# Kernel optimization log

Hardware: AMD Instinct MI355X
Metric: run time of the kernel (lower is better)

The kernel has to match this reference:

```python
import jax, jax.numpy as jnp
import numpy as np

INC, OUTC, NHEADS, KSIZE = 256, 256, 8, 5


def setup_inputs() -> dict:
    key = jax.random.key(0)
    k1, k2 = jax.random.split(key, 2)
    x = jax.random.normal(k1, (4, INC, 64, 64), dtype=jnp.float32)
    w_qkv = jax.random.normal(k2, (3 * OUTC, INC), dtype=jnp.float32) * 0.02
    b_qkv = jnp.zeros((3 * OUTC,), dtype=jnp.float32)
    return {"x": x, "w_qkv": w_qkv, "b_qkv": b_qkv}


def reference(x, w_qkv, b_qkv):
    N, Cin, H, W = x.shape
    hd = OUTC // NHEADS
    ofs = KSIZE // 2
    K2 = KSIZE * KSIZE

    # 1x1 conv == pointwise matmul over channels
    qkv = jnp.einsum('nchw,dc->ndhw', x, w_qkv) + b_qkv[None, :, None, None]
    Q = qkv[:, :OUTC]
    K = qkv[:, OUTC:2 * OUTC]
    V = qkv[:, 2 * OUTC:]

    # Zero-pad K/V; track validity so boundary softmax only spans in-bounds
    # positions (the torch code slices smaller windows at borders -> no pad
    # contribution to softmax).
    Kp = jnp.pad(K, ((0, 0), (0, 0), (ofs, ofs), (ofs, ofs)))
    Vp = jnp.pad(V, ((0, 0), (0, 0), (ofs, ofs), (ofs, ofs)))
    valid = jnp.pad(jnp.ones((H, W), dtype=bool), ((ofs, ofs), (ofs, ofs)))

    # Sliding windows via KSIZE^2 static shifted slices: [N,D,H,W,K2]
    k_win = jnp.stack([Kp[:, :, dy:dy + H, dx:dx + W]
                       for dy in range(KSIZE) for dx in range(KSIZE)], axis=-1)
    v_win = jnp.stack([Vp[:, :, dy:dy + H, dx:dx + W]
                       for dy in range(KSIZE) for dx in range(KSIZE)], axis=-1)
    m_win = jnp.stack([valid[dy:dy + H, dx:dx + W]
                       for dy in range(KSIZE) for dx in range(KSIZE)], axis=-1)  # [H,W,K2]

    qh = Q.reshape(N, NHEADS, hd, H, W)
    kh = k_win.reshape(N, NHEADS, hd, H, W, K2)
    vh = v_win.reshape(N, NHEADS, hd, H, W, K2)

    scores = jnp.einsum('ngdhw,ngdhwk->nghwk', qh, kh)          # [N,G,H,W,K2]
    scores = jnp.where(m_win[None, None], scores, -jnp.inf)
    att = jax.nn.softmax(scores, axis=-1)
    out = jnp.einsum('nghwk,ngdhwk->ngdhw', att, vh)            # [N,G,hd,H,W]
    return out.reshape(N, OUTC, H, W)
```

## Files before the change

### kernel.cpp

```cpp
#include <hip/hip_runtime.h>
#include <hip/hip_bf16.h>
#include <math.h>

#define CIN 256
#define COUT 768
#define OUTC 256
#define HH 64
#define WW 64
#define HW 4096

typedef unsigned int uint32;
typedef unsigned short ushort16;
typedef unsigned long long u64;

using short8 = __attribute__((ext_vector_type(8))) short;
using f32x4  = __attribute__((ext_vector_type(4))) float;
using hf2    = __attribute__((ext_vector_type(2))) _Float16;

__device__ inline uint32 pkbf2(float a, float b) {
    __hip_bfloat162 h = __float22bfloat162_rn(make_float2(a, b));
    union { __hip_bfloat162 h2; uint32 u; } cv; cv.h2 = h;
    return cv.u;
}
__device__ inline uint32 pkhf2(float a, float b) {
    union { _Float16 h[2]; uint32 u; } cv;
    cv.h[0] = (_Float16)a; cv.h[1] = (_Float16)b;
    return cv.u;
}
__device__ inline float dpp_xor1(float x) {
#if __has_builtin(__builtin_amdgcn_update_dpp)
    int i = __builtin_amdgcn_update_dpp(0, __float_as_int(x),
                                        0xB1, 0xF, 0xF, true);
    return __int_as_float(i);
#else
    return __shfl_xor(x, 1, 64);
#endif
}
__device__ inline float dot2acc(hf2 a, hf2 b, float c) {
#if __has_builtin(__builtin_amdgcn_fdot2)
    return __builtin_amdgcn_fdot2(a, b, c, false);
#else
    c = fmaf((float)a[0], (float)b[0], c);
    return fmaf((float)a[1], (float)b[1], c);
#endif
}

#define LDSTR 40

__global__ __launch_bounds__(256) void qkv_gemm_kernel(
    const float* __restrict__ x, const float* __restrict__ wq,
    const float* __restrict__ bq, ushort16* __restrict__ qkv)
{
    __shared__ __align__(16) char smem[32768];
    ushort16* As = (ushort16*)smem;
    ushort16* Bs = (ushort16*)smem + 128 * LDSTR;

    const int n   = blockIdx.z;
    const int d0  = blockIdx.y * 128;
    const int p0  = blockIdx.x * 128;
    const int tid = threadIdx.x;
    const int lane = tid & 63;
    const int wid  = tid >> 6;
    const int wm = wid >> 1;
    const int wn = wid & 1;

    const float* xb = x + (size_t)n * CIN * HW;

    const int arow = tid >> 2;
    const int akk  = (tid & 3) * 8;
    const float* aptr = wq + (size_t)(d0 + arow) * CIN + akk;
    const int bkg = (tid >> 6) * 8;
    const int bpg = (tid & 63) * 2;
    const float* bptr = xb + (size_t)bkg * HW + p0 + bpg;

    ushort16* awr0 = &As[arow * LDSTR + akk];
    ushort16* awr1 = &As[(arow + 64) * LDSTR + akk];
    ushort16* bwr0 = &Bs[bpg * LDSTR + bkg];
    ushort16* bwr1 = &Bs[(bpg + 1) * LDSTR + bkg];

    f32x4 acc[4][4];
    #pragma unroll
    for (int i = 0; i < 4; ++i)
        #pragma unroll
        for (int j = 0; j < 4; ++j) acc[i][j] = (f32x4){0.f, 0.f, 0.f, 0.f};

    const int lrow = lane & 15;
    const int lk   = (lane >> 4) * 8;

    float4 a0[4], a1[4];
    float2 b0[8], b1[8];

#define LOAD_SET(aS, bS, ko) do {                                         \
        aS[0] = *(const float4*)(aptr + (ko));                            \
        aS[1] = *(const float4*)(aptr + (ko) + 4);                        \
        aS[2] = *(const float4*)(aptr + (size_t)64 * CIN + (ko));         \
        aS[3] = *(const float4*)(aptr + (size_t)64 * CIN + (ko) + 4);     \
        _Pragma("unroll")                                                 \
        for (int j = 0; j < 8; ++j)                                       \
            bS[j] = *(const float2*)(bptr + (size_t)((ko) + j) * HW);     \
    } while (0)

#define WRITE_SET(aS, bS) do {                                            \
        uint32 w0 = pkbf2(aS[0].x, aS[0].y), w1 = pkbf2(aS[0].z, aS[0].w);\
        uint32 w2 = pkbf2(aS[1].x, aS[1].y), w3 = pkbf2(aS[1].z, aS[1].w);\
        *(uint4*)awr0 = make_uint4(w0, w1, w2, w3);                       \
        w0 = pkbf2(aS[2].x, aS[2].y); w1 = pkbf2(aS[2].z, aS[2].w);       \
        w2 = pkbf2(aS[3].x, aS[3].y); w3 = pkbf2(aS[3].z, aS[3].w);       \
        *(uint4*)awr1 = make_uint4(w0, w1, w2, w3);                       \
        uint4 c0, c1;                                                     \
        c0.x = pkbf2(bS[0].x, bS[1].x); c0.y = pkbf2(bS[2].x, bS[3].x);   \
        c0.z = pkbf2(bS[4].x, bS[5].x); c0.w = pkbf2(bS[6].x, bS[7].x);   \
        c1.x = pkbf2(bS[0].y, bS[1].y); c1.y = pkbf2(bS[2].y, bS[3].y);   \
        c1.z = pkbf2(bS[4].y, bS[5].y); c1.w = pkbf2(bS[6].y, bS[7].y);   \
        *(uint4*)bwr0 = c0;                                               \
        *(uint4*)bwr1 = c1;                                               \
    } while (0)

#define COMPUTE() do {                                                    \
        short8 af[4], bf[4];                                              \
        _Pragma("unroll")                                                 \
        for (int fm = 0; fm < 4; ++fm)                                    \
            af[fm] = *(const short8*)&As[(wm * 64 + fm * 16 + lrow) * LDSTR + lk]; \
        _Pragma("unroll")                                                 \
        for (int fn = 0; fn < 4; ++fn)                                    \
            bf[fn] = *(const short8*)&Bs[(wn * 64 + fn * 16 + lrow) * LDSTR + lk]; \
        _Pragma("unroll")                                                 \
        for (int fm = 0; fm < 4; ++fm)                                    \
            _Pragma("unroll")                                             \
            for (int fn = 0; fn < 4; ++fn)                                \
                acc[fm][fn] = __builtin_amdgcn_mfma_f32_16x16x32_bf16(    \
                    af[fm], bf[fn], acc[fm][fn], 0, 0, 0);                \
    } while (0)

    LOAD_SET(a0, b0, 0);
    LOAD_SET(a1, b1, 32);

    #pragma unroll 1
    for (int kt = 0; kt < 8; kt += 2) {
        __syncthreads();
        WRITE_SET(a0, b0);
        if (kt + 2 < 8) LOAD_SET(a0, b0, (kt + 2) * 32);
        __syncthreads();
        COMPUTE();

        __syncthreads();
        WRITE_SET(a1, b1);
        if (kt + 3 < 8) LOAD_SET(a1, b1, (kt + 3) * 32);
        __syncthreads();
        COMPUTE();
    }
#undef LOAD_SET
#undef WRITE_SET
#undef COMPUTE

    __syncthreads();

    u64* E = (u64*)smem + (size_t)wid * 1024;

    const int hi4 = lane >> 4;
    #pragma unroll
    for (int fm = 0; fm < 4; ++fm) {
        const int D = d0 + wm * 64 + fm * 16 + hi4 * 4;
        const float4 bias = *(const float4*)(&bq[D]);
        const int cell = fm * 2 + (hi4 >> 1);
        const int half = hi4 & 1;
        #pragma unroll
        for (int fn = 0; fn < 4; ++fn) {
            const int pl = fn * 16 + lrow;
            f32x4 v = acc[fm][fn];
            u64 pk = (u64)pkhf2(v[0] + bias.x, v[1] + bias.y)
                   | ((u64)pkhf2(v[2] + bias.z, v[3] + bias.w) << 32);
            E[pl * 16 + (cell ^ (pl & 7)) * 2 + half] = pk;
        }
    }
    const int pl4 = lane >> 2;
    const int dq  = lane & 3;
    ushort16* qn = qkv + (size_t)n * COUT * HW;
    #pragma unroll
    for (int s = 0; s < 2; ++s) {
        const int D = d0 + wm * 64 + s * 32;
        const int slot = D >> 5;
        ushort16* sb2 = qn + (size_t)slot * (HW * 32);
        #pragma unroll
        for (int g = 0; g < 4; ++g) {
            const int prow = g * 16 + pl4;
            const int c = s * 4 + dq;
            const uint4 val = *(const uint4*)&E[prow * 16 + ((c ^ (prow & 7)) * 2)];
            *(uint4*)(sb2 + (size_t)(p0 + wn * 64 + prow) * 32 + dq * 8) = val;
        }
    }
}

#define TR 4
#define TC 32
#define HR 8
#define HC 36
#define NPIX (HR*HC)

__global__ __launch_bounds__(256) void attn_kernel(
    const ushort16* __restrict__ qkv, float* __restrict__ out)
{
    __shared__ uint4 Ks[NPIX * 4];
    __shared__ uint4 Vs[NPIX * 4];

    const int n    = blockIdx.z;
    const int head = blockIdx.y;
    const int ht = blockIdx.x >> 1;
    const int wt = blockIdx.x & 1;
    const int h0 = ht * TR;
    const int w0 = wt * TC;

    const int tid  = threadIdx.x;
    const int half = tid & 1;
    const int wc   = (tid >> 1) & 31;
    const int tr   = tid >> 6;

    const int h = h0 + tr, w = w0 + wc;
    const int p = h * WW + w;

    const uint4* Kb = (const uint4*)(qkv + ((size_t)(n * 24 + 8 + head)) * HW * 32);
    const uint4* Vb = (const uint4*)(qkv + ((size_t)(n * 24 + 16 + head)) * HW * 32);

    for (int c = tid; c < 2 * NPIX * 4; c += 256) {
        const int b  = (c >= NPIX * 4);
        const int cc = c - b * NPIX * 4;
        const int pix = cc >> 2, i = cc & 3;
        const int hr = pix / HC, cw = pix - hr * HC;
        const int hh = h0 + hr - 2, ww = w0 + cw - 2;
        if (hh >= 0 && hh < HH && ww >= 0 && ww < WW) {
            const int pp = hh * WW + ww;
            const uint4 v = (b ? Vb : Kb)[(size_t)pp * 4 + i];
            const int unit = (pix * 4 + i) ^ (pix & 7);
            (b ? Vs : Ks)[unit] = v;
        }
    }

    hf2 q[8];
    {
        const uint4* Qp = (const uint4*)(qkv + (((size_t)(n * 24 + head)) * HW + p) * 32);
        union { uint4 u; hf2 h[4]; } c0, c1;
        c0.u = Qp[half * 2];
        c1.u = Qp[half * 2 + 1];
        #pragma unroll
        for (int i = 0; i < 4; ++i) { q[i] = c0.h[i]; q[4 + i] = c1.h[i]; }
    }

    __syncthreads();

    float sc[25];
    #pragma unroll
    for (int ky = 0; ky < 5; ++ky) {
        const int hh = h + ky - 2;
        const int hr = tr + ky;
        #pragma unroll
        for (int kx = 0; kx < 5; ++kx) {
            const int ww = w + kx - 2;
            float s;
            if (hh >= 0 && hh < HH && ww >= 0 && ww < WW) {
                const int pix = hr * HC + (wc + kx);
                const int u0 = (pix * 4 + half * 2)     ^ (pix & 7);
                const int u1 = (pix * 4 + half * 2 + 1) ^ (pix & 7);
                union { uint4 u; hf2 h[4]; } a, b;
                a.u = Ks[u0]; b.u = Ks[u1];
                float t = 0.f;
                t = dot2acc(q[0], a.h[0], t);
                t = dot2acc(q[1], a.h[1], t);
                t = dot2acc(q[2], a.h[2], t);
                t = dot2acc(q[3], a.h[3], t);
                t = dot2acc(q[4], b.h[0], t);
                t = dot2acc(q[5], b.h[1], t);
                t = dot2acc(q[6], b.h[2], t);
                t = dot2acc(q[7], b.h[3], t);
                s = t;
            } else {
                s = -1e30f;
            }
            sc[ky * 5 + kx] = s;
        }
    }
    #pragma unroll
    for (int k = 0; k < 25; ++k) {
        float o = dpp_xor1(sc[k]);
        sc[k] = (sc[k] <= -1e29f) ? sc[k] : sc[k] + o;
    }

    float m = sc[0];
    #pragma unroll
    for (int k = 1; k < 25; ++k) m = fmaxf(m, sc[k]);
    float sum = 0.f;
    #pragma unroll
    for (int k = 0; k < 25; ++k) {
        float e = __expf(sc[k] - m);
        sc[k] = e;
        sum += e;
    }
    const float inv = 1.f / sum;

    hf2 acch[8];
    #pragma unroll
    for (int i = 0; i < 8; ++i) acch[i] = (hf2){(_Float16)0.f, (_Float16)0.f};
    #pragma unroll
    for (int ky = 0; ky < 5; ++ky) {
        const int hh = h + ky - 2;
        if (hh < 0 || hh >= HH) continue;
        const int hr = tr + ky;
        #pragma unroll
        for (int kx = 0; kx < 5; ++kx) {
            const int ww = w + kx - 2;
            if (ww < 0 || ww >= WW) continue;
            const _Float16 af = (_Float16)sc[ky * 5 + kx];
            const hf2 ah = (hf2){af, af};
            const int pix = hr * HC + (wc + kx);
            const int u0 = (pix * 4 + half * 2)     ^ (pix & 7);
            const int u1 = (pix * 4 + half * 2 + 1) ^ (pix & 7);
            union { uint4 u; hf2 h[4]; } xv, yv;
            xv.u = Vs[u0]; yv.u = Vs[u1];
            acch[0] += ah * xv.h[0];
            acch[1] += ah * xv.h[1];
            acch[2] += ah * xv.h[2];
            acch[3] += ah * xv.h[3];
            acch[4] += ah * yv.h[0];
            acch[5] += ah * yv.h[1];
            acch[6] += ah * yv.h[2];
            acch[7] += ah * yv.h[3];
        }
    }

    float* Ob = out + ((size_t)(n * 8 + head) * 32 + half * 16) * HW + p;
    #pragma unroll
    for (int i = 0; i < 8; ++i) {
        Ob[(size_t)(2*i)   * HW] = (float)acch[i][0] * inv;
        Ob[(size_t)(2*i+1) * HW] = (float)acch[i][1] * inv;
    }
}

extern "C" void kernel_launch(void* const* d_in, const int* in_sizes, int n_in,
                              void* d_out, int out_size, void* d_ws, size_t ws_size,
                              hipStream_t stream) {
    const float* x  = (const float*)d_in[0];
    const float* wq = (const float*)d_in[1];
    const float* bq = (const float*)d_in[2];
    float* out = (float*)d_out;
    ushort16* qkv = (ushort16*)d_ws;

    dim3 g1(HW / 128, COUT / 128, 4);
    qkv_gemm_kernel<<<g1, 256, 0, stream>>>(x, wq, bq, qkv);

    dim3 g2(32, 8, 4);
    attn_kernel<<<g2, 256, 0, stream>>>(qkv, out);
}
```

Before: 41.49 us.

## Pre-convert weights to bf16 and double-buffer B tile in QKV GEMM

Adds a small kernel that converts the fp32 QKV weights to bf16 in workspace on every call. The GEMM then loads A fragments directly from global memory into registers instead of staging them through LDS. It also double-buffers the B (activation) tile in LDS, cutting barriers per k-step from two to one. The aim is less LDS traffic, less sync and less in-loop conversion work, at the cost of an extra kernel launch and uncoalesced, unshared per-wave global loads of A.

```diff
diff --git a/kernel.cpp b/kernel.cpp
--- a/kernel.cpp
+++ b/kernel.cpp
@@ -45,15 +45,25 @@
 #endif
 }
 
+__global__ __launch_bounds__(256) void cvt_w_kernel(
+    const float* __restrict__ wq, ushort16* __restrict__ wb)
+{
+    const int i = (blockIdx.x * 256 + threadIdx.x) * 8;
+    float4 a = *(const float4*)&wq[i];
+    float4 b = *(const float4*)&wq[i + 4];
+    *(uint4*)&wb[i] = make_uint4(pkbf2(a.x, a.y), pkbf2(a.z, a.w),
+                                 pkbf2(b.x, b.y), pkbf2(b.z, b.w));
+}
+
 #define LDSTR 40
 
 __global__ __launch_bounds__(256) void qkv_gemm_kernel(
-    const float* __restrict__ x, const float* __restrict__ wq,
+    const float* __restrict__ x, const ushort16* __restrict__ wb,
     const float* __restrict__ bq, ushort16* __restrict__ qkv)
 {
     __shared__ __align__(16) char smem[32768];
-    ushort16* As = (ushort16*)smem;
-    ushort16* Bs = (ushort16*)smem + 128 * LDSTR;
+    ushort16* Bs0 = (ushort16*)smem;
+    ushort16* Bs1 = (ushort16*)smem + 128 * LDSTR;
 
     const int n   = blockIdx.z;
     const int d0  = blockIdx.y * 128;
@@ -66,91 +76,86 @@
 
     const float* xb = x + (size_t)n * CIN * HW;
 
-    const int arow = tid >> 2;
-    const int akk  = (tid & 3) * 8;
-    const float* aptr = wq + (size_t)(d0 + arow) * CIN + akk;
+    const int lrow = lane & 15;
+    const int lk   = (lane >> 4) * 8;
+
+    const ushort16* ap[4];
+    #pragma unroll
+    for (int fm = 0; fm < 4; ++fm)
+        ap[fm] = wb + (size_t)(d0 + wm * 64 + fm * 16 + lrow) * CIN + lk;
+
     const int bkg = (tid >> 6) * 8;
     const int bpg = (tid & 63) * 2;
     const float* bptr = xb + (size_t)bkg * HW + p0 + bpg;
 
-    ushort16* awr0 = &As[arow * LDSTR + akk];
-    ushort16* awr1 = &As[(arow + 64) * LDSTR + akk];
-    ushort16* bwr0 = &Bs[bpg * LDSTR + bkg];
-    ushort16* bwr1 = &Bs[(bpg + 1) * LDSTR + bkg];
-
     f32x4 acc[4][4];
     #pragma unroll
     for (int i = 0; i < 4; ++i)
         #pragma unroll
         for (int j = 0; j < 4; ++j) acc[i][j] = (f32x4){0.f, 0.f, 0.f, 0.f};
 
-    const int lrow = lane & 15;
-    const int lk   = (lane >> 4) * 8;
-
-    float4 a0[4], a1[4];
-    float2 b0[8], b1[8];
-
-#define LOAD_SET(aS, bS, ko) do {                                         \
-        aS[0] = *(const float4*)(aptr + (ko));                            \
-        aS[1] = *(const float4*)(aptr + (ko) + 4);                        \
-        aS[2] = *(const float4*)(aptr + (size_t)64 * CIN + (ko));         \
-        aS[3] = *(const float4*)(aptr + (size_t)64 * CIN + (ko) + 4);     \
+    float2 breg[8];
+
+#define LOADB(ko) do {                                                    \
         _Pragma("unroll")                                                 \
         for (int j = 0; j < 8; ++j)                                       \
-            bS[j] = *(const float2*)(bptr + (size_t)((ko) + j) * HW);     \
+            breg[j] = *(const float2*)(bptr + (size_t)((ko) + j) * HW);   \
     } while (0)
 
-#define WRITE_SET(aS, bS) do {                                            \
-        uint32 w0 = pkbf2(aS[0].x, aS[0].y), w1 = pkbf2(aS[0].z, aS[0].w);\
-        uint32 w2 = pkbf2(aS[1].x, aS[1].y), w3 = pkbf2(aS[1].z, aS[1].w);\
-        *(uint4*)awr0 = make_uint4(w0, w1, w2, w3);                       \
-        w0 = pkbf2(aS[2].x, aS[2].y); w1 = pkbf2(aS[2].z, aS[2].w);       \
-        w2 = pkbf2(aS[3].x, aS[3].y); w3 = pkbf2(aS[3].z, aS[3].w);       \
-        *(uint4*)awr1 = make_uint4(w0, w1, w2, w3);                       \
+#define WRITEB(Bsb) do {                                                  \
         uint4 c0, c1;                                                     \
-        c0.x = pkbf2(bS[0].x, bS[1].x); c0.y = pkbf2(bS[2].x, bS[3].x);   \
-        c0.z = pkbf2(bS[4].x, bS[5].x); c0.w = pkbf2(bS[6].x, bS[7].x);   \
-        c1.x = pkbf2(bS[0].y, bS[1].y); c1.y = pkbf2(bS[2].y, bS[3].y);   \
-        c1.z = pkbf2(bS[4].y, bS[5].y); c1.w = pkbf2(bS[6].y, bS[7].y);   \
-        *(uint4*)bwr0 = c0;                                               \
-        *(uint4*)bwr1 = c1;                                               \
+        c0.x = pkbf2(breg[0].x, breg[1].x); c0.y = pkbf2(breg[2].x, breg[3].x); \
+        c0.z = pkbf2(breg[4].x, breg[5].x); c0.w = pkbf2(breg[6].x, breg[7].x); \
+        c1.x = pkbf2(breg[0].y, breg[1].y); c1.y = pkbf2(breg[2].y, breg[3].y); \
+        c1.z = pkbf2(breg[4].y, breg[5].y); c1.w = pkbf2(breg[6].y, breg[7].y); \
+        *(uint4*)&(Bsb)[bpg * LDSTR + bkg]       = c0;                    \
+        *(uint4*)&(Bsb)[(bpg + 1) * LDSTR + bkg] = c1;                    \
     } while (0)
 
-#define COMPUTE() do {                                                    \
-        short8 af[4], bf[4];                                              \
+#define LOADA(dst, ko) do {                                               \
         _Pragma("unroll")                                                 \
         for (int fm = 0; fm < 4; ++fm)                                    \
-            af[fm] = *(const short8*)&As[(wm * 64 + fm * 16 + lrow) * LDSTR + lk]; \
+            dst[fm] = *(const short8*)(ap[fm] + (ko));                    \
+    } while (0)
+
+#define COMPUTE(Bsb, afr) do {                                            \
+        short8 bf[4];                                                     \
         _Pragma("unroll")                                                 \
         for (int fn = 0; fn < 4; ++fn)                                    \
-            bf[fn] = *(const short8*)&Bs[(wn * 64 + fn * 16 + lrow) * LDSTR + lk]; \
+            bf[fn] = *(const short8*)&(Bsb)[(wn * 64 + fn * 16 + lrow) * LDSTR + lk]; \
         _Pragma("unroll")                                                 \
         for (int fm = 0; fm < 4; ++fm)                                    \
             _Pragma("unroll")                                             \
             for (int fn = 0; fn < 4; ++fn)                                \
                 acc[fm][fn] = __builtin_amdgcn_mfma_f32_16x16x32_bf16(    \
-                    af[fm], bf[fn], acc[fm][fn], 0, 0, 0);                \
+                    afr[fm], bf[fn], acc[fm][fn], 0, 0, 0);               \
     } while (0)
 
-    LOAD_SET(a0, b0, 0);
-    LOAD_SET(a1, b1, 32);
+    short8 aX[4], aY[4];
+
+    LOADB(0);
+    LOADA(aX, 0);
+    WRITEB(Bs0);
+    LOADB(32);
+    __syncthreads();
 
     #pragma unroll 1
     for (int kt = 0; kt < 8; kt += 2) {
+        LOADA(aY, (kt + 1) * 32);
+        COMPUTE(Bs0, aX);
+        WRITEB(Bs1);
+        if (kt + 2 < 8) LOADB((kt + 2) * 32);
         __syncthreads();
-        WRITE_SET(a0, b0);
-        if (kt + 2 < 8) LOAD_SET(a0, b0, (kt + 2) * 32);
+
+        if (kt + 2 < 8) LOADA(aX, (kt + 2) * 32);
+        COMPUTE(Bs1, aY);
+        if (kt + 2 < 8) WRITEB(Bs0);
+        if (kt + 3 < 8) LOADB((kt + 3) * 32);
         __syncthreads();
-        COMPUTE();
-
-        __syncthreads();
-        WRITE_SET(a1, b1);
-        if (kt + 3 < 8) LOAD_SET(a1, b1, (kt + 3) * 32);
-        __syncthreads();
-        COMPUTE();
-    }
-#undef LOAD_SET
-#undef WRITE_SET
+    }
+#undef LOADB
+#undef WRITEB
+#undef LOADA
 #undef COMPUTE
 
     __syncthreads();
@@ -341,10 +346,14 @@
     const float* wq = (const float*)d_in[1];
     const float* bq = (const float*)d_in[2];
     float* out = (float*)d_out;
+
     ushort16* qkv = (ushort16*)d_ws;
+    ushort16* wbf = (ushort16*)((char*)d_ws + (32u << 20));
+
+    cvt_w_kernel<<<96, 256, 0, stream>>>(wq, wbf);
 
     dim3 g1(HW / 128, COUT / 128, 4);
-    qkv_gemm_kernel<<<g1, 256, 0, stream>>>(x, wq, bq, qkv);
+    qkv_gemm_kernel<<<g1, 256, 0, stream>>>(x, wbf, bq, qkv);
 
     dim3 g2(32, 8, 4);
     attn_kernel<<<g2, 256, 0, stream>>>(qkv, out);
```

Result: slower. 51.81 us (+24.9%).
